# Kernel tuning notes

Hardware: AMD Instinct MI355X
Metric: run time of the kernel (lower is better)

The kernel has to match this reference:

```python
import jax, jax.numpy as jnp
import numpy as np

B, A, C, M = 32, 8400, 80, 32
TOP_K, ALPHA, BETA, EPS = 13, 1.0, 6.0, 1e-9


def _boxes(key, shape):
    # valid xyxy boxes in a 640x640 image
    u = jax.random.uniform(key, shape, jnp.float32)
    xy = u[..., :2] * 640.0
    wh = u[..., 2:] * 128.0 + 2.0
    return jnp.concatenate([xy, xy + wh], axis=-1)


def setup_inputs() -> dict:
    key = jax.random.key(0)
    k = jax.random.split(key, 6)
    pd_scores = jax.random.uniform(k[0], (B, A, C), jnp.float32)
    pd_bboxes = _boxes(k[1], (B, A, 4))
    anc_points = jax.random.uniform(k[2], (A, 2), jnp.float32) * 640.0
    gt_labels = jax.random.randint(k[3], (B, M, 1), 0, C, jnp.int32)
    gt_bboxes = _boxes(k[4], (B, M, 4))
    mask_gt = (jax.random.uniform(k[5], (B, M, 1)) < 0.8).astype(jnp.float32)
    return {"pd_scores": pd_scores, "pd_bboxes": pd_bboxes, "anc_points": anc_points,
            "gt_labels": gt_labels, "gt_bboxes": gt_bboxes, "mask_gt": mask_gt}


def _assign(pd_scores, pd_bboxes, anc_points, gt_labels, gt_bboxes, mask_gt):
    b, a, nc = pd_scores.shape
    m = gt_bboxes.shape[1]
    dtype = pd_scores.dtype

    # --- candidate anchors inside each GT box: (B, M, A) ---
    lt, rb = gt_bboxes[..., :2], gt_bboxes[..., 2:]                  # (B,M,2)
    deltas = jnp.concatenate([anc_points[None, None] - lt[:, :, None],
                              rb[:, :, None] - anc_points[None, None]], axis=-1)  # (B,M,A,4)
    mask_in_gts = (deltas.min(-1) > EPS).astype(dtype)               # (B,M,A)
    gt_mask = (mask_in_gts * mask_gt) > 0                            # bool (B,M,A)

    # --- classification score of each anchor for its GT's class ---
    labels = gt_labels[..., 0].astype(jnp.int32)                     # (B,M)
    scores_tc = jnp.swapaxes(pd_scores, 1, 2)                        # (B,C,A)
    idx = jnp.broadcast_to(labels[:, :, None], (b, m, a))
    bbox_scores = jnp.take_along_axis(scores_tc, idx, axis=1)        # (B,M,A)
    bbox_scores = jnp.where(gt_mask, bbox_scores, 0.0)

    # --- pairwise IoU gt x pred: (B,M,A) ---
    lt_i = jnp.maximum(gt_bboxes[:, :, None, :2], pd_bboxes[:, None, :, :2])
    rb_i = jnp.minimum(gt_bboxes[:, :, None, 2:], pd_bboxes[:, None, :, 2:])
    wh = jnp.clip(rb_i - lt_i, 0.0)
    inter = wh[..., 0] * wh[..., 1]
    area_g = ((gt_bboxes[..., 2] - gt_bboxes[..., 0]) * (gt_bboxes[..., 3] - gt_bboxes[..., 1]))[:, :, None]
    area_p = ((pd_bboxes[..., 2] - pd_bboxes[..., 0]) * (pd_bboxes[..., 3] - pd_bboxes[..., 1]))[:, None, :]
    iou = inter / (area_g + area_p - inter + EPS)
    overlaps = jnp.clip(jnp.where(gt_mask, iou, 0.0), 0.0)

    align_metric = bbox_scores ** ALPHA * overlaps ** BETA           # (B,M,A)

    # --- top-k over anchors, dedup via scatter-add counts ---
    tk_vals, tk_idx = jax.lax.top_k(align_metric, TOP_K)             # (B,M,K)
    tk_mask = jnp.broadcast_to(mask_gt > 0, (b, m, TOP_K))
    tk_idx = jnp.where(tk_mask, tk_idx, 0)
    bi = jnp.arange(b)[:, None, None]
    mi = jnp.arange(m)[None, :, None]
    counts = jnp.zeros((b, m, a), jnp.int32).at[bi, mi, tk_idx].add(1)
    mask_top_k = jnp.where(counts > 1, 0, counts).astype(dtype)

    mask_pos = mask_top_k * mask_in_gts * mask_gt                    # (B,M,A)
    fg_mask = mask_pos.sum(1)                                        # (B,A)

    # --- resolve anchors assigned to multiple GTs by max IoU ---
    # (always applied; identical to torch's conditional branch when no conflicts)
    mask_multi = jnp.broadcast_to(fg_mask[:, None, :] > 1, (b, m, a))
    max_ov_idx = jnp.argmax(overlaps, axis=1)                        # (B,A)
    is_max = (max_ov_idx[:, None, :] == jnp.arange(m)[None, :, None]).astype(dtype)
    mask_pos = jnp.where(mask_multi, is_max, mask_pos)
    fg_mask = mask_pos.sum(1)

    # --- gather targets ---
    tgt_idx = jnp.argmax(mask_pos, axis=1)                           # (B,A)
    tgt_labels = jnp.clip(jnp.take_along_axis(labels, tgt_idx, axis=1), 0)  # (B,A)
    tgt_bboxes = jnp.take_along_axis(gt_bboxes, jnp.broadcast_to(tgt_idx[:, :, None], (b, a, 4)), axis=1)

    one_hot = (tgt_labels[..., None] == jnp.arange(nc)).astype(dtype)  # (B,A,C)
    target_scores = one_hot * (fg_mask > 0)[..., None].astype(dtype)

    # --- normalize scores by aligned metric ---
    am = align_metric * mask_pos
    pos_am = am.max(-1, keepdims=True)                               # (B,M,1)
    pos_ov = (overlaps * mask_pos).max(-1, keepdims=True)            # (B,M,1)
    norm = (am * pos_ov / (pos_am + EPS)).max(axis=1)[..., None]     # (B,A,1)
    target_scores = target_scores * norm

    return tgt_bboxes, target_scores, fg_mask > 0


def reference(pd_scores, pd_bboxes, anc_points, gt_labels, gt_bboxes, mask_gt):
    return _assign(pd_scores, pd_bboxes, anc_points, gt_labels, gt_bboxes, mask_gt)
```

## Files before the change

### kernel.cpp

```cpp
#include <hip/hip_runtime.h>

#define Bq 32
#define Aq 8400
#define Cq 80
#define Mq 32
#define TOPK 13
#define CAP 512
#define EPSq 1e-9f

__device__ __forceinline__ bool better(float v1, int i1, float v2, int i2) {
    return (v1 > v2) || ((v1 == v2) && (i1 < i2));
}

__device__ __forceinline__ float iou4(float4 g, float4 p, float garea) {
    float ix1 = fmaxf(g.x, p.x), iy1 = fmaxf(g.y, p.y);
    float ix2 = fminf(g.z, p.z), iy2 = fminf(g.w, p.w);
    float iw = fmaxf(ix2 - ix1, 0.f), ih = fmaxf(iy2 - iy1, 0.f);
    float inter = iw * ih;
    float parea = (p.z - p.x) * (p.w - p.y);
    return inter / (((garea + parea) - inter) + EPSq);
}

__device__ __forceinline__ float in_min4(float ax, float ay, float4 g) {
    return fminf(fminf(ax - g.x, ay - g.y), fminf(g.z - ax, g.w - ay));
}

__device__ __forceinline__ void ins13(float (&val)[TOPK], int (&idx)[TOPK], float al, int a) {
    if (better(al, a, val[TOPK - 1], idx[TOPK - 1])) {
        #pragma unroll
        for (int k = TOPK - 1; k >= 1; --k) {
            bool bk   = better(val[k],     idx[k],     al, a);
            bool bkm1 = better(val[k - 1], idx[k - 1], al, a);
            val[k] = bk ? val[k] : (bkm1 ? al : val[k - 1]);
            idx[k] = bk ? idx[k] : (bkm1 ? a  : idx[k - 1]);
        }
        bool b0 = better(val[0], idx[0], al, a);
        val[0] = b0 ? val[0] : al;
        idx[0] = b0 ? idx[0] : a;
    }
}

__global__ __launch_bounds__(256) void k_build(
    const float* __restrict__ pd_scores, const float* __restrict__ pd_bboxes,
    const float* __restrict__ anc, const int* __restrict__ gt_labels,
    const float* __restrict__ gt_bboxes, const float* __restrict__ mask_gt,
    unsigned int* __restrict__ zero_region,
    int* __restrict__ winners)
{
    int m = blockIdx.x, b = blockIdx.y;
    int t = threadIdx.x, lane = t & 63;

    int gid = (b * Mq + m) * 256 + t;
    if (gid < 2 * Bq * Mq) zero_region[gid] = 0u;

    __shared__ int   s_n;
    __shared__ int   s_list[CAP];
    __shared__ float s_val[CAP];

    if (mask_gt[b * Mq + m] <= 0.f) {
        if (t < TOPK) winners[(b * Mq + m) * TOPK + t] = -1;
        return;
    }

    if (t == 0) s_n = 0;
    __syncthreads();

    float4 gb = ((const float4*)gt_bboxes)[b * Mq + m];
    float garea = (gb.z - gb.x) * (gb.w - gb.y);

    for (int a = t; a < Aq; a += 256) {
        float2 ap = ((const float2*)anc)[a];
        bool in = in_min4(ap.x, ap.y, gb) > EPSq;
        unsigned long long bal = __ballot(in);
        if (bal) {
            int rank = __popcll(bal & ((1ull << lane) - 1ull));
            int leader = __ffsll(bal) - 1;
            int base = 0;
            if (lane == leader) base = atomicAdd(&s_n, (int)__popcll(bal));
            base = __shfl(base, leader);
            int pos = base + rank;
            if (in && pos < CAP) s_list[pos] = a;
        }
    }
    __syncthreads();

    int n = s_n < CAP ? s_n : CAP;
    int lbl = gt_labels[b * Mq + m];
    for (int e = t; e < n; e += 256) {
        int a = s_list[e];
        float4 pb = ((const float4*)pd_bboxes)[(size_t)b * Aq + a];
        float ov = fmaxf(iou4(gb, pb, garea), 0.f);
        float sc = pd_scores[((size_t)b * Aq + a) * Cq + lbl];
        float o2 = ov * ov;
        s_val[e] = sc * (o2 * o2 * o2);
    }
    __syncthreads();

    if (t >= 64) return;

    float val[TOPK]; int idx[TOPK];
    #pragma unroll
    for (int k = 0; k < TOPK; k++) { val[k] = -1.f; idx[k] = 0x7fffffff; }

    {
        float2 apl = ((const float2*)anc)[lane];
        if (!(in_min4(apl.x, apl.y, gb) > EPSq)) ins13(val, idx, 0.f, lane);
    }
    for (int e = lane; e < n; e += 64) ins13(val, idx, s_val[e], s_list[e]);

    int win_i = 0x7fffffff;
    #pragma unroll
    for (int r = 0; r < TOPK; ++r) {
        float bv = val[0]; int bi = idx[0];
        #pragma unroll
        for (int off = 1; off < 64; off <<= 1) {
            float ovv = __shfl_xor(bv, off);
            int   oii = __shfl_xor(bi, off);
            if (better(ovv, oii, bv, bi)) { bv = ovv; bi = oii; }
        }
        if (lane == r) win_i = bi;
        if (idx[0] == bi) {
            #pragma unroll
            for (int k = 0; k < TOPK - 1; ++k) { val[k] = val[k + 1]; idx[k] = idx[k + 1]; }
            val[TOPK - 1] = -1.f; idx[TOPK - 1] = 0x7fffffff;
        }
    }
    if (lane < TOPK) {
        int outv = -1;
        if (win_i < Aq) {
            float2 ap = ((const float2*)anc)[win_i];
            if (in_min4(ap.x, ap.y, gb) > EPSq) outv = win_i;
        }
        winners[(b * Mq + m) * TOPK + lane] = outv;
    }
}

__global__ __launch_bounds__(256) void k_resolve(
    const float* __restrict__ pd_scores, const float* __restrict__ pd_bboxes,
    const float* __restrict__ anc, const int* __restrict__ gt_labels,
    const float* __restrict__ gt_bboxes, const float* __restrict__ mask_gt,
    const int* __restrict__ winners,
    unsigned int* __restrict__ finalmask, float* __restrict__ asel,
    unsigned int* __restrict__ pos_am, unsigned int* __restrict__ pos_ov,
    float* __restrict__ out_bboxes, float* __restrict__ out_fg)
{
    int b = blockIdx.y;
    int a0 = blockIdx.x * 256;
    int t = threadIdx.x;

    __shared__ unsigned int smask[256];
    smask[t] = 0u;
    __syncthreads();

    for (int e = t; e < Mq * TOPK; e += 256) {
        int a = winners[(size_t)b * Mq * TOPK + e];
        if (a >= a0 && a < a0 + 256) {
            int m = e / TOPK;
            atomicOr(&smask[a - a0], 1u << m);
        }
    }
    __syncthreads();

    int a = a0 + t;
    if (a >= Aq) return;
    size_t i = (size_t)b * Aq + a;

    unsigned int w = smask[t];
    float4 pb = ((const float4*)pd_bboxes)[i];
    float2 ap = ((const float2*)anc)[a];

    if (__popc(w) > 1) {
        float bv = -1.f; int bj = 0;
        for (int mm = 0; mm < Mq; mm++) {
            float4 g = ((const float4*)gt_bboxes)[b * Mq + mm];
            float ov = 0.f;
            if (in_min4(ap.x, ap.y, g) > EPSq && mask_gt[b * Mq + mm] > 0.f) {
                float garea = (g.z - g.x) * (g.w - g.y);
                ov = fmaxf(iou4(g, pb, garea), 0.f);
            }
            if (ov > bv) { bv = ov; bj = mm; }
        }
        w = 1u << bj;
    }
    finalmask[i] = w;

    int j = w ? (__ffs(w) - 1) : 0;
    float4 g = ((const float4*)gt_bboxes)[b * Mq + j];
    ((float4*)out_bboxes)[i] = g;
    out_fg[i] = w ? 1.f : 0.f;

    if (w) {
        float al = 0.f, ov = 0.f;
        if (in_min4(ap.x, ap.y, g) > EPSq && mask_gt[b * Mq + j] > 0.f) {
            float garea = (g.z - g.x) * (g.w - g.y);
            ov = fmaxf(iou4(g, pb, garea), 0.f);
            float sc = pd_scores[i * Cq + gt_labels[b * Mq + j]];
            float o2 = ov * ov;
            al = sc * (o2 * o2 * o2);
        }
        asel[i] = al;
        atomicMax(&pos_am[b * Mq + j], __float_as_uint(al));
        atomicMax(&pos_ov[b * Mq + j], __float_as_uint(ov));
    }
}

__global__ __launch_bounds__(256) void k_scores(
    const int* __restrict__ gt_labels,
    const unsigned int* __restrict__ finalmask,
    const float* __restrict__ asel,
    const unsigned int* __restrict__ pos_am, const unsigned int* __restrict__ pos_ov,
    float* __restrict__ out_scores)
{
    int i4 = blockIdx.x * 256 + threadIdx.x;
    if (i4 >= Bq * Aq * Cq / 4) return;
    int i = i4 * 4;
    int c0 = i % Cq;
    int ba = i / Cq;
    unsigned int w = finalmask[ba];
    float4 o = make_float4(0.f, 0.f, 0.f, 0.f);
    if (w) {
        int b = ba / Aq;
        int j = __ffs(w) - 1;
        int lb = gt_labels[b * Mq + j];
        if (lb >= c0 && lb < c0 + 4) {
            float pam = __uint_as_float(pos_am[b * Mq + j]);
            float pov = __uint_as_float(pos_ov[b * Mq + j]);
            float nv = asel[ba] * pov / (pam + EPSq);
            o.x = (lb == c0    ) ? nv : 0.f;
            o.y = (lb == c0 + 1) ? nv : 0.f;
            o.z = (lb == c0 + 2) ? nv : 0.f;
            o.w = (lb == c0 + 3) ? nv : 0.f;
        }
    }
    ((float4*)out_scores)[i4] = o;
}

extern "C" void kernel_launch(void* const* d_in, const int* in_sizes, int n_in,
                              void* d_out, int out_size, void* d_ws, size_t ws_size,
                              hipStream_t stream) {
    const float* pd_scores = (const float*)d_in[0];
    const float* pd_bboxes = (const float*)d_in[1];
    const float* anc       = (const float*)d_in[2];
    const int*   gt_labels = (const int*)d_in[3];
    const float* gt_bboxes = (const float*)d_in[4];
    const float* mask_gt   = (const float*)d_in[5];

    float* out_bboxes = (float*)d_out;
    float* out_scores = out_bboxes + (size_t)Bq * Aq * 4;
    float* out_fg     = out_scores + (size_t)Bq * Aq * Cq;

    char* ws = (char*)d_ws;
    const size_t BA4 = (size_t)Bq * Aq * 4;
    const size_t BM4 = (size_t)Bq * Mq * 4;
    unsigned int* pos_am    = (unsigned int*)ws;  ws += BM4;
    unsigned int* pos_ov    = (unsigned int*)ws;  ws += BM4;
    unsigned int* finalmask = (unsigned int*)ws;  ws += BA4;
    float*        asel      = (float*)ws;         ws += BA4;
    int*          winners   = (int*)ws;           ws += (size_t)Bq * Mq * TOPK * 4;

    k_build<<<dim3(Mq, Bq), 256, 0, stream>>>(
        pd_scores, pd_bboxes, anc, gt_labels, gt_bboxes, mask_gt,
        pos_am , winners);

    k_resolve<<<dim3((Aq + 255) / 256, Bq), 256, 0, stream>>>(
        pd_scores, pd_bboxes, anc, gt_labels, gt_bboxes, mask_gt,
        winners, finalmask, asel, pos_am, pos_ov, out_bboxes, out_fg);

    k_scores<<<(Bq * Aq * Cq / 4 + 255) / 256, 256, 0, stream>>>(
        gt_labels, finalmask, asel, pos_am, pos_ov, out_scores);
}
```

Before: 190.7 us.

## Fuse resolve and score kernels by recomputing per-batch positives in each block

Merges k_resolve and k_scores into a single k_write kernel. Each block rebuilds the full per-batch anchor mask in shared memory (Aq words) from the winners list. It resolves multi-GT conflicts and computes per-GT max align and overlap redundantly for only the ~416 winner anchors, then writes bboxes, fg and the dense score rows directly. This removes a kernel launch, the global finalmask/asel/pos_am/pos_ov round trips and the global atomics. The costs are ~33KB of shared memory per block, which may limit occupancy, and the winner-processing work duplicated in every block.

```diff
diff --git a/kernel.cpp b/kernel.cpp
--- a/kernel.cpp
+++ b/kernel.cpp
@@ -6,6 +6,7 @@
 #define Mq 32
 #define TOPK 13
 #define CAP 512
+#define NW (Mq * TOPK)
 #define EPSq 1e-9f
 
 __device__ __forceinline__ bool better(float v1, int i1, float v2, int i2) {
@@ -44,14 +45,10 @@
     const float* __restrict__ pd_scores, const float* __restrict__ pd_bboxes,
     const float* __restrict__ anc, const int* __restrict__ gt_labels,
     const float* __restrict__ gt_bboxes, const float* __restrict__ mask_gt,
-    unsigned int* __restrict__ zero_region,
     int* __restrict__ winners)
 {
     int m = blockIdx.x, b = blockIdx.y;
     int t = threadIdx.x, lane = t & 63;
-
-    int gid = (b * Mq + m) * 256 + t;
-    if (gid < 2 * Bq * Mq) zero_region[gid] = 0u;
 
     __shared__ int   s_n;
     __shared__ int   s_list[CAP];
@@ -135,104 +132,133 @@
     }
 }
 
-__global__ __launch_bounds__(256) void k_resolve(
+__global__ __launch_bounds__(256) void k_write(
     const float* __restrict__ pd_scores, const float* __restrict__ pd_bboxes,
     const float* __restrict__ anc, const int* __restrict__ gt_labels,
     const float* __restrict__ gt_bboxes, const float* __restrict__ mask_gt,
     const int* __restrict__ winners,
-    unsigned int* __restrict__ finalmask, float* __restrict__ asel,
-    unsigned int* __restrict__ pos_am, unsigned int* __restrict__ pos_ov,
-    float* __restrict__ out_bboxes, float* __restrict__ out_fg)
+    float* __restrict__ out_bboxes, float* __restrict__ out_scores,
+    float* __restrict__ out_fg)
 {
     int b = blockIdx.y;
     int a0 = blockIdx.x * 256;
     int t = threadIdx.x;
 
-    __shared__ unsigned int smask[256];
-    smask[t] = 0u;
-    __syncthreads();
-
-    for (int e = t; e < Mq * TOPK; e += 256) {
-        int a = winners[(size_t)b * Mq * TOPK + e];
-        if (a >= a0 && a < a0 + 256) {
-            int m = e / TOPK;
-            atomicOr(&smask[a - a0], 1u << m);
-        }
-    }
-    __syncthreads();
-
-    int a = a0 + t;
-    if (a >= Aq) return;
-    size_t i = (size_t)b * Aq + a;
-
-    unsigned int w = smask[t];
-    float4 pb = ((const float4*)pd_bboxes)[i];
-    float2 ap = ((const float2*)anc)[a];
-
-    if (__popc(w) > 1) {
-        float bv = -1.f; int bj = 0;
-        for (int mm = 0; mm < Mq; mm++) {
-            float4 g = ((const float4*)gt_bboxes)[b * Mq + mm];
-            float ov = 0.f;
-            if (in_min4(ap.x, ap.y, g) > EPSq && mask_gt[b * Mq + mm] > 0.f) {
-                float garea = (g.z - g.x) * (g.w - g.y);
-                ov = fmaxf(iou4(g, pb, garea), 0.f);
+    __shared__ unsigned int smask[Aq];
+    __shared__ unsigned int s_am[Mq], s_ov[Mq];
+    __shared__ float4 sgb[Mq];
+    __shared__ int    slbl[Mq];
+    __shared__ int    smv[Mq];
+    __shared__ float  snv[256];
+    __shared__ int    slb[256];
+
+    if (t < Mq) {
+        sgb[t]  = ((const float4*)gt_bboxes)[b * Mq + t];
+        slbl[t] = gt_labels[b * Mq + t];
+        smv[t]  = (mask_gt[b * Mq + t] > 0.f) ? 1 : 0;
+        s_am[t] = 0u; s_ov[t] = 0u;
+    }
+    for (int a = t; a < Aq; a += 256) smask[a] = 0u;
+    __syncthreads();
+
+    for (int e = t; e < NW; e += 256) {
+        int a = winners[(size_t)b * NW + e];
+        if (a >= 0) atomicOr(&smask[a], 1u << (e / TOPK));
+    }
+    __syncthreads();
+
+    int ea[2]; unsigned int ewm[2];
+    #pragma unroll
+    for (int r = 0; r < 2; ++r) {
+        int e = t + r * 256;
+        int a = (e < NW) ? winners[(size_t)b * NW + e] : -1;
+        ea[r] = a;
+        ewm[r] = (a >= 0) ? smask[a] : 0u;
+    }
+    __syncthreads();
+
+    #pragma unroll
+    for (int r = 0; r < 2; ++r) {
+        int a = ea[r];
+        if (a < 0) continue;
+        unsigned int w = ewm[r];
+        float4 pb = ((const float4*)pd_bboxes)[(size_t)b * Aq + a];
+        float2 ap = ((const float2*)anc)[a];
+        if (__popc(w) > 1) {
+            float bv = -1.f; int bj = 0;
+            for (int mm = 0; mm < Mq; mm++) {
+                float4 g = sgb[mm];
+                float ov = 0.f;
+                if (in_min4(ap.x, ap.y, g) > EPSq && smv[mm]) {
+                    float garea = (g.z - g.x) * (g.w - g.y);
+                    ov = fmaxf(iou4(g, pb, garea), 0.f);
+                }
+                if (ov > bv) { bv = ov; bj = mm; }
             }
-            if (ov > bv) { bv = ov; bj = mm; }
-        }
-        w = 1u << bj;
-    }
-    finalmask[i] = w;
-
-    int j = w ? (__ffs(w) - 1) : 0;
-    float4 g = ((const float4*)gt_bboxes)[b * Mq + j];
-    ((float4*)out_bboxes)[i] = g;
-    out_fg[i] = w ? 1.f : 0.f;
-
-    if (w) {
+            w = 1u << bj;
+            smask[a] = w;
+        }
+        int j = __ffs(w) - 1;
         float al = 0.f, ov = 0.f;
-        if (in_min4(ap.x, ap.y, g) > EPSq && mask_gt[b * Mq + j] > 0.f) {
+        float4 g = sgb[j];
+        if (in_min4(ap.x, ap.y, g) > EPSq && smv[j]) {
             float garea = (g.z - g.x) * (g.w - g.y);
             ov = fmaxf(iou4(g, pb, garea), 0.f);
-            float sc = pd_scores[i * Cq + gt_labels[b * Mq + j]];
+            float sc = pd_scores[((size_t)b * Aq + a) * Cq + slbl[j]];
             float o2 = ov * ov;
             al = sc * (o2 * o2 * o2);
         }
-        asel[i] = al;
-        atomicMax(&pos_am[b * Mq + j], __float_as_uint(al));
-        atomicMax(&pos_ov[b * Mq + j], __float_as_uint(ov));
-    }
-}
-
-__global__ __launch_bounds__(256) void k_scores(
-    const int* __restrict__ gt_labels,
-    const unsigned int* __restrict__ finalmask,
-    const float* __restrict__ asel,
-    const unsigned int* __restrict__ pos_am, const unsigned int* __restrict__ pos_ov,
-    float* __restrict__ out_scores)
-{
-    int i4 = blockIdx.x * 256 + threadIdx.x;
-    if (i4 >= Bq * Aq * Cq / 4) return;
-    int i = i4 * 4;
-    int c0 = i % Cq;
-    int ba = i / Cq;
-    unsigned int w = finalmask[ba];
-    float4 o = make_float4(0.f, 0.f, 0.f, 0.f);
-    if (w) {
-        int b = ba / Aq;
-        int j = __ffs(w) - 1;
-        int lb = gt_labels[b * Mq + j];
-        if (lb >= c0 && lb < c0 + 4) {
-            float pam = __uint_as_float(pos_am[b * Mq + j]);
-            float pov = __uint_as_float(pos_ov[b * Mq + j]);
-            float nv = asel[ba] * pov / (pam + EPSq);
-            o.x = (lb == c0    ) ? nv : 0.f;
-            o.y = (lb == c0 + 1) ? nv : 0.f;
-            o.z = (lb == c0 + 2) ? nv : 0.f;
-            o.w = (lb == c0 + 3) ? nv : 0.f;
-        }
-    }
-    ((float4*)out_scores)[i4] = o;
+        atomicMax(&s_am[j], __float_as_uint(al));
+        atomicMax(&s_ov[j], __float_as_uint(ov));
+    }
+    __syncthreads();
+
+    int a = a0 + t;
+    {
+        float nv = 0.f; int lb = -1;
+        if (a < Aq) {
+            size_t i = (size_t)b * Aq + a;
+            unsigned int w = smask[a];
+            int j = w ? (__ffs(w) - 1) : 0;
+            ((float4*)out_bboxes)[i] = sgb[j];
+            out_fg[i] = w ? 1.f : 0.f;
+            if (w) {
+                lb = slbl[j];
+                float2 ap = ((const float2*)anc)[a];
+                float4 pb = ((const float4*)pd_bboxes)[i];
+                float al = 0.f;
+                float4 g = sgb[j];
+                if (in_min4(ap.x, ap.y, g) > EPSq && smv[j]) {
+                    float garea = (g.z - g.x) * (g.w - g.y);
+                    float ov = fmaxf(iou4(g, pb, garea), 0.f);
+                    float sc = pd_scores[i * Cq + lb];
+                    float o2 = ov * ov;
+                    al = sc * (o2 * o2 * o2);
+                }
+                float pam = __uint_as_float(s_am[j]);
+                float pov = __uint_as_float(s_ov[j]);
+                nv = al * pov / (pam + EPSq);
+            }
+        }
+        snv[t] = nv;
+        slb[t] = lb;
+    }
+    __syncthreads();
+
+    const int C4 = Cq / 4;
+    int nrow = Aq - a0; if (nrow > 256) nrow = 256;
+    for (int idx = t; idx < nrow * C4; idx += 256) {
+        int row = idx / C4, c4 = idx - row * C4;
+        float4 o = make_float4(0.f, 0.f, 0.f, 0.f);
+        int lbr = slb[row];
+        if (lbr >= 0 && (lbr >> 2) == c4) {
+            float v = snv[row];
+            int p = lbr & 3;
+            if (p == 0) o.x = v; else if (p == 1) o.y = v;
+            else if (p == 2) o.z = v; else o.w = v;
+        }
+        ((float4*)out_scores)[((size_t)b * Aq + a0 + row) * C4 + c4] = o;
+    }
 }
 
 extern "C" void kernel_launch(void* const* d_in, const int* in_sizes, int n_in,
@@ -249,23 +275,12 @@
     float* out_scores = out_bboxes + (size_t)Bq * Aq * 4;
     float* out_fg     = out_scores + (size_t)Bq * Aq * Cq;
 
-    char* ws = (char*)d_ws;
-    const size_t BA4 = (size_t)Bq * Aq * 4;
-    const size_t BM4 = (size_t)Bq * Mq * 4;
-    unsigned int* pos_am    = (unsigned int*)ws;  ws += BM4;
-    unsigned int* pos_ov    = (unsigned int*)ws;  ws += BM4;
-    unsigned int* finalmask = (unsigned int*)ws;  ws += BA4;
-    float*        asel      = (float*)ws;         ws += BA4;
-    int*          winners   = (int*)ws;           ws += (size_t)Bq * Mq * TOPK * 4;
+    int* winners = (int*)d_ws;
 
     k_build<<<dim3(Mq, Bq), 256, 0, stream>>>(
-        pd_scores, pd_bboxes, anc, gt_labels, gt_bboxes, mask_gt,
-        pos_am , winners);
-
-    k_resolve<<<dim3((Aq + 255) / 256, Bq), 256, 0, stream>>>(
-        pd_scores, pd_bboxes, anc, gt_labels, gt_bboxes, mask_gt,
-        winners, finalmask, asel, pos_am, pos_ov, out_bboxes, out_fg);
-
-    k_scores<<<(Bq * Aq * Cq / 4 + 255) / 256, 256, 0, stream>>>(
-        gt_labels, finalmask, asel, pos_am, pos_ov, out_scores);
-}
+        pd_scores, pd_bboxes, anc, gt_labels, gt_bboxes, mask_gt, winners);
+
+    k_write<<<dim3((Aq + 255) / 256, Bq), 256, 0, stream>>>(
+        pd_scores, pd_bboxes, anc, gt_labels, gt_bboxes, mask_gt, winners,
+        out_bboxes, out_scores, out_fg);
+}
```

Measured after the change: 190.3 us. No clear change (-0.2%).
